# Kernel tuning notes

Measured on AMD Instinct MI355X. Metric: run time of the kernel, lower is better.

Reference implementation:

```python
import jax, jax.numpy as jnp
import numpy as np

B, N, D = 4, 4096, 512
E = 4 * D            # expanded_dim = 2048
TAIL = E // 2        # tail_dim = 1024
HALF = TAIL // 2     # mt_half = 512
HEAD = E - TAIL      # head_dim = 1024
EPS_RMS = 1e-6
EPS_NORM = 1e-12


def setup_inputs() -> dict:
    key = jax.random.key(0)
    k = jax.random.split(key, 6)
    x = jax.random.normal(k[0], (B, N, D), dtype=jnp.float32)
    g = jnp.ones((D,), dtype=jnp.float32)                                   # RMSNorm gain
    W1 = jax.random.normal(k[1], (D, E), dtype=jnp.float32) * 0.02          # Enricher linear
    b1 = jnp.zeros((E,), dtype=jnp.float32)
    V = jax.random.normal(k[2], (N, N), dtype=jnp.float32) * 0.02           # learned positional matrix slice
    bias = jnp.zeros((HALF,), dtype=jnp.float32)                            # contextualizer bias
    Wf = jax.random.normal(k[3], (HEAD + HALF, D), dtype=jnp.float32) * 0.02  # Fuser linear (no bias)
    return {"x": x, "g": g, "W1": W1, "b1": b1, "V": V, "bias": bias, "Wf": Wf}


def reference(x, g, W1, b1, V, bias, Wf):
    # RMSNorm
    xn = x * jax.lax.rsqrt(jnp.mean(jnp.square(x), axis=-1, keepdims=True) + EPS_RMS) * g
    # Enricher: relu(linear)^2
    enriched = jnp.square(jax.nn.relu(xn @ W1 + b1))                        # [B, N, E]
    head = enriched[..., :HEAD]                                             # [B, N, HEAD]
    tail = enriched[..., HEAD:]                                             # [B, N, TAIL]
    # Contextualizer
    x_left = tail[..., :HALF]
    x_right = tail[..., HALF:]
    nrm = jnp.sqrt(jnp.sum(jnp.square(x_right), axis=-1, keepdims=True))
    xr_n = x_right / jnp.maximum(nrm, EPS_NORM)                             # F.normalize, p=2
    cos = jnp.einsum('bnd,bmd->bnm', xr_n, xr_n)                            # [B, N, N] cosine sim
    weighted = V[None, :, :] * cos                                          # elementwise learned V
    ctx = jnp.einsum('bnm,bmd->bnd', weighted, xr_n)                        # chunked-path bmm uses x_right_norm
    ctx = jax.nn.sigmoid(ctx + bias)
    gated = x_left * ctx                                                    # [B, N, HALF]
    # Fuser + residual
    out = jnp.concatenate([head, gated], axis=-1) @ Wf                      # [B, N, D]
    return x + out
```

## Files before the change

### kernel.cpp

```cpp
#include <hip/hip_runtime.h>
#include <hip/hip_bf16.h>
#include <stdint.h>

typedef unsigned short u16;
typedef unsigned long long u64;
typedef __attribute__((ext_vector_type(8))) short bf16x8;
typedef __attribute__((ext_vector_type(4))) float f32x4;
typedef __attribute__((ext_vector_type(16))) float f32x16;
typedef __attribute__((ext_vector_type(4))) unsigned int u32x4;
typedef __attribute__((ext_vector_type(4))) unsigned short u16x4;

#define DEV static __device__ __forceinline__

DEV u16 f2bf(float f){
  __hip_bfloat16 h = __float2bfloat16(f);
  return __builtin_bit_cast(u16, h);
}
DEV float bf2f(u16 v){
  unsigned u = ((unsigned)v) << 16;
  return __builtin_bit_cast(float, u);
}

DEV void async_lds16(const void* g, void* l){
  __builtin_amdgcn_global_load_lds(
      (const __attribute__((address_space(1))) unsigned int*)g,
      (__attribute__((address_space(3))) unsigned int*)l, 16, 0, 0);
}

DEV f32x4 mfma16(bf16x8 a, bf16x8 b, f32x4 c){
  return __builtin_amdgcn_mfma_f32_16x16x32_bf16(a, b, c, 0, 0, 0);
}
DEV f32x16 mfma32(bf16x8 a, bf16x8 b, f32x16 c){
  return __builtin_amdgcn_mfma_f32_32x32x16_bf16(a, b, c, 0, 0, 0);
}

__global__ __launch_bounds__(64) void k_rms(const float* __restrict__ x,
                                            const float* __restrict__ g,
                                            u16* __restrict__ xn){
  const int row = blockIdx.x;
  const int l = threadIdx.x;
  const float* xr = x + (size_t)row * 512 + l * 8;
  f32x4 a = *(const f32x4*)xr;
  f32x4 c = *(const f32x4*)(xr + 4);
  float s = a[0]*a[0]+a[1]*a[1]+a[2]*a[2]+a[3]*a[3]
          + c[0]*c[0]+c[1]*c[1]+c[2]*c[2]+c[3]*c[3];
  #pragma unroll
  for (int off = 32; off >= 1; off >>= 1) s += __shfl_xor(s, off);
  float sc = rsqrtf(s * (1.f/512.f) + 1e-6f);
  f32x4 g0 = *(const f32x4*)&g[l*8];
  f32x4 g1 = *(const f32x4*)&g[l*8+4];
  u32x4 o;
  o[0] = (unsigned)f2bf(a[0]*sc*g0[0]) | ((unsigned)f2bf(a[1]*sc*g0[1]) << 16);
  o[1] = (unsigned)f2bf(a[2]*sc*g0[2]) | ((unsigned)f2bf(a[3]*sc*g0[3]) << 16);
  o[2] = (unsigned)f2bf(c[0]*sc*g1[0]) | ((unsigned)f2bf(c[1]*sc*g1[1]) << 16);
  o[3] = (unsigned)f2bf(c[2]*sc*g1[2]) | ((unsigned)f2bf(c[3]*sc*g1[3]) << 16);
  *(u32x4*)&xn[(size_t)row*512 + l*8] = o;
}

__global__ __launch_bounds__(64) void k_norm(const float* __restrict__ xr_in,
                                             u16* __restrict__ xrn){
  const int row = blockIdx.x;
  const int l = threadIdx.x;
  const float* xr = xr_in + (size_t)row * 512 + l * 8;
  f32x4 a = *(const f32x4*)xr;
  f32x4 c = *(const f32x4*)(xr + 4);
  float s = a[0]*a[0]+a[1]*a[1]+a[2]*a[2]+a[3]*a[3]
          + c[0]*c[0]+c[1]*c[1]+c[2]*c[2]+c[3]*c[3];
  #pragma unroll
  for (int off = 32; off >= 1; off >>= 1) s += __shfl_xor(s, off);
  float sc = 1.f / fmaxf(sqrtf(s), 1e-12f);
  u32x4 o;
  o[0] = (unsigned)f2bf(a[0]*sc) | ((unsigned)f2bf(a[1]*sc) << 16);
  o[1] = (unsigned)f2bf(a[2]*sc) | ((unsigned)f2bf(a[3]*sc) << 16);
  o[2] = (unsigned)f2bf(c[0]*sc) | ((unsigned)f2bf(c[1]*sc) << 16);
  o[3] = (unsigned)f2bf(c[2]*sc) | ((unsigned)f2bf(c[3]*sc) << 16);
  *(u32x4*)&xrn[(size_t)row*512 + l*8] = o;
}

__global__ __launch_bounds__(256) void k_castV(const float* __restrict__ V,
                                               u16* __restrict__ Vb){
  size_t i = ((size_t)blockIdx.x * 256 + threadIdx.x) * 8;
  f32x4 a = *(const f32x4*)&V[i];
  f32x4 c = *(const f32x4*)&V[i+4];
  u32x4 o;
  o[0] = (unsigned)f2bf(a[0]) | ((unsigned)f2bf(a[1]) << 16);
  o[1] = (unsigned)f2bf(a[2]) | ((unsigned)f2bf(a[3]) << 16);
  o[2] = (unsigned)f2bf(c[0]) | ((unsigned)f2bf(c[1]) << 16);
  o[3] = (unsigned)f2bf(c[2]) | ((unsigned)f2bf(c[3]) << 16);
  *(u32x4*)&Vb[i] = o;
}

__global__ __launch_bounds__(256) void k_tr32(const float* __restrict__ in,
                                              u16* __restrict__ out, int R, int C){
  __shared__ float tile[32][33];
  const int t = threadIdx.x;
  const int r = t >> 3;
  const int c4 = (t & 7) << 2;
  const int r0 = blockIdx.y << 5, c0 = blockIdx.x << 5;
  f32x4 v = *(const f32x4*)&in[(size_t)(r0 + r) * C + c0 + c4];
  tile[r][c4+0]=v[0]; tile[r][c4+1]=v[1]; tile[r][c4+2]=v[2]; tile[r][c4+3]=v[3];
  __syncthreads();
  u64 o =
      (u64)f2bf(tile[c4+0][r])
    | ((u64)f2bf(tile[c4+1][r]) << 16)
    | ((u64)f2bf(tile[c4+2][r]) << 32)
    | ((u64)f2bf(tile[c4+3][r]) << 48);
  *(u64*)&out[(size_t)(c0 + r) * R + r0 + c4] = o;
}

__global__ __launch_bounds__(256) void k_trb(const u16* __restrict__ in,
                                             u16* __restrict__ out, int R, int C){
  __shared__ u16 tile[32][40];
  const int t = threadIdx.x;
  const int r = t >> 3;
  const int c4 = (t & 7) << 2;
  const size_t bb = (size_t)blockIdx.z * R * C;
  const int r0 = blockIdx.y << 5, c0 = blockIdx.x << 5;
  u64 v = *(const u64*)&in[bb + (size_t)(r0 + r)*C + c0 + c4];
  tile[r][c4+0]=(u16)v; tile[r][c4+1]=(u16)(v>>16);
  tile[r][c4+2]=(u16)(v>>32); tile[r][c4+3]=(u16)(v>>48);
  __syncthreads();
  u64 o =
      (u64)tile[c4+0][r]
    | ((u64)tile[c4+1][r] << 16)
    | ((u64)tile[c4+2][r] << 32)
    | ((u64)tile[c4+3][r] << 48);
  *(u64*)&out[bb + (size_t)(c0 + r) * R + r0 + c4] = o;
}

__global__ __launch_bounds__(256) void k_gemm1(const u16* __restrict__ A,
                                               const u16* __restrict__ Bt,
                                               const float* __restrict__ b1,
                                               u16* __restrict__ head,
                                               float* __restrict__ xleft,
                                               float* __restrict__ xright){
  __shared__ u16 As[128*32];
  __shared__ u16 Bs[128*32];
  const int t = threadIdx.x;
  const int l = t & 63;
  const int w = t >> 6;
  const int wr = w >> 1, wc = w & 1;
  const int m0 = blockIdx.x << 7;
  const int n0 = blockIdx.y << 7;
  const int ra = t >> 2;
  const int kb = (t & 3) << 3;
  const int lr = l & 15, lh = l >> 4;
  f32x4 acc[4][4];
  #pragma unroll
  for (int i=0;i<4;i++)
    #pragma unroll
    for (int j=0;j<4;j++)
      #pragma unroll
      for (int r=0;r<4;r++) acc[i][j][r] = 0.f;
  for (int k0 = 0; k0 < 512; k0 += 32){
    async_lds16(A  + (size_t)(m0 + ra)*512      + k0 + kb, &As[t*8]);
    async_lds16(A  + (size_t)(m0 + 64 + ra)*512 + k0 + kb, &As[2048 + t*8]);
    async_lds16(Bt + (size_t)(n0 + ra)*512      + k0 + kb, &Bs[t*8]);
    async_lds16(Bt + (size_t)(n0 + 64 + ra)*512 + k0 + kb, &Bs[2048 + t*8]);
    __syncthreads();
    bf16x8 af[4], bfr[4];
    #pragma unroll
    for (int i=0;i<4;i++){
      af[i]  = *(const bf16x8*)&As[(wr*64 + i*16 + lr)*32 + lh*8];
      bfr[i] = *(const bf16x8*)&Bs[(wc*64 + i*16 + lr)*32 + lh*8];
    }
    #pragma unroll
    for (int i=0;i<4;i++)
      #pragma unroll
      for (int j=0;j<4;j++)
        acc[i][j] = mfma16(af[i], bfr[j], acc[i][j]);
    __syncthreads();
  }
  #pragma unroll
  for (int i=0;i<4;i++){
    #pragma unroll
    for (int j=0;j<4;j++){
      int c = n0 + wc*64 + j*16 + lr;
      float bb = b1[c];
      #pragma unroll
      for (int r=0;r<4;r++){
        int m = m0 + wr*64 + i*16 + lh*4 + r;
        float v = acc[i][j][r] + bb;
        v = v > 0.f ? v*v : 0.f;
        if (c < 1024)      head[(size_t)m*1024 + c] = f2bf(v);
        else if (c < 1536) xleft[(size_t)m*512 + (c - 1024)] = v;
        else               xright[(size_t)m*512 + (c - 1536)] = v;
      }
    }
  }
}

__global__ __launch_bounds__(256) void k_gemm3(const u16* __restrict__ head,
                                               const u16* __restrict__ gated,
                                               const u16* __restrict__ Wft,
                                               const float* __restrict__ x,
                                               float* __restrict__ out){
  __shared__ u16 As[128*32];
  __shared__ u16 Bs[128*32];
  const int t = threadIdx.x;
  const int l = t & 63;
  const int w = t >> 6;
  const int wr = w >> 1, wc = w & 1;
  const int m0 = blockIdx.x << 7;
  const int n0 = blockIdx.y << 7;
  const int ra = t >> 2;
  const int kb = (t & 3) << 3;
  const int lr = l & 15, lh = l >> 4;
  f32x4 acc[4][4];
  #pragma unroll
  for (int i=0;i<4;i++)
    #pragma unroll
    for (int j=0;j<4;j++)
      #pragma unroll
      for (int r=0;r<4;r++) acc[i][j][r] = 0.f;
  for (int k0 = 0; k0 < 1536; k0 += 32){
    const u16* sa; size_t lda; int kk;
    if (k0 < 1024){ sa = head;  lda = 1024; kk = k0; }
    else          { sa = gated; lda = 512;  kk = k0 - 1024; }
    async_lds16(sa + (size_t)(m0 + ra)*lda      + kk + kb, &As[t*8]);
    async_lds16(sa + (size_t)(m0 + 64 + ra)*lda + kk + kb, &As[2048 + t*8]);
    async_lds16(Wft + (size_t)(n0 + ra)*1536      + k0 + kb, &Bs[t*8]);
    async_lds16(Wft + (size_t)(n0 + 64 + ra)*1536 + k0 + kb, &Bs[2048 + t*8]);
    __syncthreads();
    bf16x8 af[4], bfr[4];
    #pragma unroll
    for (int i=0;i<4;i++){
      af[i]  = *(const bf16x8*)&As[(wr*64 + i*16 + lr)*32 + lh*8];
      bfr[i] = *(const bf16x8*)&Bs[(wc*64 + i*16 + lr)*32 + lh*8];
    }
    #pragma unroll
    for (int i=0;i<4;i++)
      #pragma unroll
      for (int j=0;j<4;j++)
        acc[i][j] = mfma16(af[i], bfr[j], acc[i][j]);
    __syncthreads();
  }
  #pragma unroll
  for (int i=0;i<4;i++){
    #pragma unroll
    for (int j=0;j<4;j++){
      int c = n0 + wc*64 + j*16 + lr;
      #pragma unroll
      for (int r=0;r<4;r++){
        int m = m0 + wr*64 + i*16 + lh*4 + r;
        size_t gi = (size_t)m*512 + c;
        out[gi] = x[gi] + acc[i][j][r];
      }
    }
  }
}

__global__ __launch_bounds__(512, 2) void k_attn(const u16* __restrict__ xrn,
                                                 const u16* __restrict__ xrT,
                                                 const u16* __restrict__ Vb,
                                                 const float* __restrict__ bias,
                                                 const float* __restrict__ xleft,
                                                 u16* __restrict__ gated){
  __shared__ char smem[153600];
  char* km = smem;
  char* tq = smem + 65536;
  char* ps = smem + 131072;
  char* pb = smem + 149504;
  const int t = threadIdx.x;
  const int l = t & 63, w = t >> 6;
  const int wr = w >> 2, ks = w & 3, wc = (w >> 1) & 1, kq2 = w & 1;
  const int lo = l & 31, hi = l >> 5;
  const int bid = blockIdx.x;
  const int b  = (bid & 7) >> 1;
  const int n0 = ((((bid >> 3) << 1) | (bid & 1))) << 6;
  const u16* xb  = xrn + (size_t)b * (4096*512);
  const u16* xTb = xrT + (size_t)b * (512*4096);

  bf16x8 areg[8];
  {
    const u16* apt = xb + (size_t)(n0 + wr*32 + lo)*512 + ks*128 + hi*8;
    #pragma unroll
    for (int kq = 0; kq < 8; ++kq) areg[kq] = *(const bf16x8*)(apt + kq*16);
  }
  f32x16 acc[8];
  #pragma unroll
  for (int i = 0; i < 8; ++i)
    #pragma unroll
    for (int j = 0; j < 16; ++j) acc[i][j] = 0.f;

  const int prf = t >> 3;
  const int pc4 = (t & 7) << 2;
  const int wrr = prf >> 5, prr = prf & 31;

  #pragma unroll
  for (int c = 0; c < 4; ++c){
    int off = (c*512 + t)*16;
    int row = off >> 10, colb = off & 1023;
    async_lds16(xb + (size_t)row*512 + ((colb ^ ((row&15)<<4)) >> 1), km + off);
    int r   = off >> 8;
    int lg  = (off & 255) ^ ((r & 15) << 4);
    int q   = lg >> 6;
    int mc  = (lg & 63) >> 1;
    async_lds16(xTb + (size_t)(q*128 + r)*4096 + mc, tq + off);
  }
  __syncthreads();

  int cur = 0;
  for (int it = 0; it < 128; ++it){
    const int m0 = it << 5;
    u16x4 vv = *(const u16x4*)&Vb[(size_t)(n0 + prf)*4096 + m0 + pc4];
    if (it < 127){
      const int m1 = m0 + 32;
      const int nb = (cur ^ 1) * 32768;
      #pragma unroll
      for (int c = 0; c < 4; ++c){
        int off = (c*512 + t)*16;
        int row = off >> 10, colb = off & 1023;
        async_lds16(xb + (size_t)(m1 + row)*512 + ((colb ^ ((row&15)<<4)) >> 1),
                    km + nb + off);
        int r   = off >> 8;
        int lg  = (off & 255) ^ ((r & 15) << 4);
        int q   = lg >> 6;
        int mc  = (lg & 63) >> 1;
        async_lds16(xTb + (size_t)(q*128 + r)*4096 + m1 + mc, tq + nb + off);
      }
    }
    f32x16 S0, S1;
    #pragma unroll
    for (int j = 0; j < 16; ++j){ S0[j] = 0.f; S1[j] = 0.f; }
    {
      const char* kbp = km + cur*32768 + lo*1024;
      const int swk = (lo & 15) << 4;
      __builtin_amdgcn_s_setprio(1);
      #pragma unroll
      for (int kq = 0; kq < 8; kq += 2){
        bf16x8 b0 = *(const bf16x8*)(kbp + ((ks*256 + kq*32 + hi*16) ^ swk));
        bf16x8 b1 = *(const bf16x8*)(kbp + ((ks*256 + (kq+1)*32 + hi*16) ^ swk));
        S0 = mfma32(areg[kq],   b0, S0);
        S1 = mfma32(areg[kq+1], b1, S1);
      }
      __builtin_amdgcn_s_setprio(0);
    }
    {
      char* pw = ps + ((wr*4 + ks)*32)*72 + lo*2;
      #pragma unroll
      for (int rg = 0; rg < 16; ++rg){
        int prow = (rg & 3) + 8*(rg >> 2) + 4*hi;
        *(u16*)(pw + prow*72) = f2bf(S0[rg] + S1[rg]);
      }
    }
    asm volatile("s_waitcnt lgkmcnt(0)" ::: "memory");
    __builtin_amdgcn_s_barrier();
    __builtin_amdgcn_sched_barrier(0);
    {
      float s0=0.f, s1=0.f, s2=0.f, s3=0.f;
      #pragma unroll
      for (int k2 = 0; k2 < 4; ++k2){
        u16x4 pv = *(const u16x4*)(ps + (((wrr*4 + k2)*32 + prr)*36 + pc4)*2);
        s0 += bf2f(pv[0]); s1 += bf2f(pv[1]); s2 += bf2f(pv[2]); s3 += bf2f(pv[3]);
      }
      u64 po = (u64)f2bf(s0 * bf2f(vv[0]))
             | ((u64)f2bf(s1 * bf2f(vv[1])) << 16)
             | ((u64)f2bf(s2 * bf2f(vv[2])) << 32)
             | ((u64)f2bf(s3 * bf2f(vv[3])) << 48);
      *(u64*)(pb + prf*72 + pc4*2) = po;
    }
    asm volatile("s_waitcnt lgkmcnt(0)" ::: "memory");
    __builtin_amdgcn_s_barrier();
    __builtin_amdgcn_sched_barrier(0);
    {
      bf16x8 pa = *(const bf16x8*)(pb + (wr*32 + lo)*72 + kq2*32 + hi*16);
      const char* tb = tq + cur*32768;
      __builtin_amdgcn_s_setprio(1);
      #pragma unroll
      for (int ds = 0; ds < 8; ++ds){
        int d = wc*256 + ds*32 + lo;
        int r = d & 127, q = d >> 7;
        bf16x8 bfr = *(const bf16x8*)(tb + r*256 +
                       ((q*64 + kq2*32 + hi*16) ^ ((r & 15) << 4)));
        acc[ds] = mfma32(pa, bfr, acc[ds]);
      }
      __builtin_amdgcn_s_setprio(0);
    }
    __syncthreads();
    cur ^= 1;
  }

  float* red = (float*)smem;
  const int rbase = (wr*2 + wc) * 8192;
  if (kq2 == 1){
    #pragma unroll
    for (int ds = 0; ds < 8; ++ds)
      #pragma unroll
      for (int rg = 0; rg < 16; ++rg)
        red[rbase + (ds*16 + rg)*64 + l] = acc[ds][rg];
  }
  __syncthreads();
  if (kq2 == 0){
    #pragma unroll
    for (int ds = 0; ds < 8; ++ds){
      const int d = wc*256 + ds*32 + lo;
      const float bs = bias[d];
      #pragma unroll
      for (int rg = 0; rg < 16; ++rg){
        int row = n0 + wr*32 + (rg & 3) + 8*(rg >> 2) + 4*hi;
        float v = acc[ds][rg] + red[rbase + (ds*16 + rg)*64 + l] + bs;
        v = 1.f / (1.f + __expf(-v));
        size_t gi = (size_t)(b*4096 + row)*512 + d;
        gated[gi] = f2bf(xleft[gi] * v);
      }
    }
  }
}

extern "C" void kernel_launch(void* const* d_in, const int* in_sizes, int n_in,
                              void* d_out, int out_size, void* d_ws, size_t ws_size,
                              hipStream_t stream){
  const float* x    = (const float*)d_in[0];
  const float* g    = (const float*)d_in[1];
  const float* W1   = (const float*)d_in[2];
  const float* b1   = (const float*)d_in[3];
  const float* V    = (const float*)d_in[4];
  const float* bias = (const float*)d_in[5];
  const float* Wf   = (const float*)d_in[6];
  float* out = (float*)d_out;

  char* ws = (char*)d_ws;
  const size_t MB = 1024u*1024u;
  u16*   xn     = (u16*)  (ws + 0*MB);
  u16*   W1t    = (u16*)  (ws + 16*MB);
  u16*   Vbf    = (u16*)  (ws + 0*MB);
  u16*   Wft    = (u16*)  (ws + 32*MB);
  u16*   head   = (u16*)  (ws + 34*MB);
  float* xleft  = (float*)(ws + 66*MB);
  float* xright = (float*)(ws + 98*MB);
  u16*   gated  = (u16*)  (ws + 98*MB);
  u16*   xrn    = (u16*)  (ws + 130*MB);
  u16*   xrT    = (u16*)  (ws + 146*MB);

  k_rms  <<<dim3(16384),      dim3(64),  0, stream>>>(x, g, xn);
  k_tr32 <<<dim3(64, 16),     dim3(256), 0, stream>>>(W1, W1t, 512, 2048);
  k_tr32 <<<dim3(16, 48),     dim3(256), 0, stream>>>(Wf, Wft, 1536, 512);
  k_gemm1<<<dim3(128, 16),    dim3(256), 0, stream>>>(xn, W1t, b1, head, xleft, xright);
  k_castV<<<dim3(8192),       dim3(256), 0, stream>>>(V, Vbf);
  k_norm <<<dim3(16384),      dim3(64),  0, stream>>>(xright, xrn);
  k_trb  <<<dim3(16, 128, 4), dim3(256), 0, stream>>>(xrn, xrT, 4096, 512);
  k_attn <<<dim3(256),        dim3(512), 0, stream>>>(xrn, xrT, Vbf, bias, xleft, gated);
  k_gemm3<<<dim3(128, 4),     dim3(256), 0, stream>>>(head, gated, Wft, x, out);
}
```

Measured before the change: 426.0 us.

## Fuse V bf16 cast into attention kernel and drop setprio hints

Removes the separate k_castV pass that turned the 4096x4096 V matrix into bf16, and has k_attn read fp32 V directly, multiplying in fp32 before rounding. This saves one launch and a full read/write of V, but the attention kernel now loads twice as many bytes of V per iteration. It also replaces the HIP bf16 conversion with a hand-written round-to-nearest-even bit trick, drops the s_setprio hints around the MFMA loops, compacts the workspace layout, and enlarges the shared buffer slightly.

```diff
diff --git a/kernel.cpp b/kernel.cpp
--- a/kernel.cpp
+++ b/kernel.cpp
@@ -1,5 +1,4 @@
 #include <hip/hip_runtime.h>
-#include <hip/hip_bf16.h>
 #include <stdint.h>
 
 typedef unsigned short u16;
@@ -13,8 +12,9 @@
 #define DEV static __device__ __forceinline__
 
 DEV u16 f2bf(float f){
-  __hip_bfloat16 h = __float2bfloat16(f);
-  return __builtin_bit_cast(u16, h);
+  unsigned u = __builtin_bit_cast(unsigned, f);
+  u += 0x7fffu + ((u >> 16) & 1u);
+  return (u16)(u >> 16);
 }
 DEV float bf2f(u16 v){
   unsigned u = ((unsigned)v) << 16;
@@ -75,19 +75,6 @@
   o[2] = (unsigned)f2bf(c[0]*sc) | ((unsigned)f2bf(c[1]*sc) << 16);
   o[3] = (unsigned)f2bf(c[2]*sc) | ((unsigned)f2bf(c[3]*sc) << 16);
   *(u32x4*)&xrn[(size_t)row*512 + l*8] = o;
-}
-
-__global__ __launch_bounds__(256) void k_castV(const float* __restrict__ V,
-                                               u16* __restrict__ Vb){
-  size_t i = ((size_t)blockIdx.x * 256 + threadIdx.x) * 8;
-  f32x4 a = *(const f32x4*)&V[i];
-  f32x4 c = *(const f32x4*)&V[i+4];
-  u32x4 o;
-  o[0] = (unsigned)f2bf(a[0]) | ((unsigned)f2bf(a[1]) << 16);
-  o[1] = (unsigned)f2bf(a[2]) | ((unsigned)f2bf(a[3]) << 16);
-  o[2] = (unsigned)f2bf(c[0]) | ((unsigned)f2bf(c[1]) << 16);
-  o[3] = (unsigned)f2bf(c[2]) | ((unsigned)f2bf(c[3]) << 16);
-  *(u32x4*)&Vb[i] = o;
 }
 
 __global__ __launch_bounds__(256) void k_tr32(const float* __restrict__ in,
@@ -252,11 +239,11 @@
 
 __global__ __launch_bounds__(512, 2) void k_attn(const u16* __restrict__ xrn,
                                                  const u16* __restrict__ xrT,
-                                                 const u16* __restrict__ Vb,
+                                                 const float* __restrict__ V,
                                                  const float* __restrict__ bias,
                                                  const float* __restrict__ xleft,
                                                  u16* __restrict__ gated){
-  __shared__ char smem[153600];
+  __shared__ char smem[154624];
   char* km = smem;
   char* tq = smem + 65536;
   char* ps = smem + 131072;
@@ -303,7 +290,7 @@
   int cur = 0;
   for (int it = 0; it < 128; ++it){
     const int m0 = it << 5;
-    u16x4 vv = *(const u16x4*)&Vb[(size_t)(n0 + prf)*4096 + m0 + pc4];
+    f32x4 vf = *(const f32x4*)&V[(size_t)(n0 + prf)*4096 + m0 + pc4];
     if (it < 127){
       const int m1 = m0 + 32;
       const int nb = (cur ^ 1) * 32768;
@@ -326,7 +313,6 @@
     {
       const char* kbp = km + cur*32768 + lo*1024;
       const int swk = (lo & 15) << 4;
-      __builtin_amdgcn_s_setprio(1);
       #pragma unroll
       for (int kq = 0; kq < 8; kq += 2){
         bf16x8 b0 = *(const bf16x8*)(kbp + ((ks*256 + kq*32 + hi*16) ^ swk));
@@ -334,7 +320,6 @@
         S0 = mfma32(areg[kq],   b0, S0);
         S1 = mfma32(areg[kq+1], b1, S1);
       }
-      __builtin_amdgcn_s_setprio(0);
     }
     {
       char* pw = ps + ((wr*4 + ks)*32)*72 + lo*2;
@@ -354,10 +339,10 @@
         u16x4 pv = *(const u16x4*)(ps + (((wrr*4 + k2)*32 + prr)*36 + pc4)*2);
         s0 += bf2f(pv[0]); s1 += bf2f(pv[1]); s2 += bf2f(pv[2]); s3 += bf2f(pv[3]);
       }
-      u64 po = (u64)f2bf(s0 * bf2f(vv[0]))
-             | ((u64)f2bf(s1 * bf2f(vv[1])) << 16)
-             | ((u64)f2bf(s2 * bf2f(vv[2])) << 32)
-             | ((u64)f2bf(s3 * bf2f(vv[3])) << 48);
+      u64 po = (u64)f2bf(s0 * vf[0])
+             | ((u64)f2bf(s1 * vf[1]) << 16)
+             | ((u64)f2bf(s2 * vf[2]) << 32)
+             | ((u64)f2bf(s3 * vf[3]) << 48);
       *(u64*)(pb + prf*72 + pc4*2) = po;
     }
     asm volatile("s_waitcnt lgkmcnt(0)" ::: "memory");
@@ -366,7 +351,6 @@
     {
       bf16x8 pa = *(const bf16x8*)(pb + (wr*32 + lo)*72 + kq2*32 + hi*16);
       const char* tb = tq + cur*32768;
-      __builtin_amdgcn_s_setprio(1);
       #pragma unroll
       for (int ds = 0; ds < 8; ++ds){
         int d = wc*256 + ds*32 + lo;
@@ -375,7 +359,6 @@
                        ((q*64 + kq2*32 + hi*16) ^ ((r & 15) << 4)));
         acc[ds] = mfma32(pa, bfr, acc[ds]);
       }
-      __builtin_amdgcn_s_setprio(0);
     }
     __syncthreads();
     cur ^= 1;
@@ -424,22 +407,20 @@
   const size_t MB = 1024u*1024u;
   u16*   xn     = (u16*)  (ws + 0*MB);
   u16*   W1t    = (u16*)  (ws + 16*MB);
-  u16*   Vbf    = (u16*)  (ws + 0*MB);
-  u16*   Wft    = (u16*)  (ws + 32*MB);
-  u16*   head   = (u16*)  (ws + 34*MB);
-  float* xleft  = (float*)(ws + 66*MB);
-  float* xright = (float*)(ws + 98*MB);
-  u16*   gated  = (u16*)  (ws + 98*MB);
-  u16*   xrn    = (u16*)  (ws + 130*MB);
-  u16*   xrT    = (u16*)  (ws + 146*MB);
+  u16*   Wft    = (u16*)  (ws + 18*MB);
+  u16*   head   = (u16*)  (ws + 20*MB);
+  float* xleft  = (float*)(ws + 52*MB);
+  float* xright = (float*)(ws + 84*MB);
+  u16*   gated  = (u16*)  (ws + 84*MB);
+  u16*   xrn    = (u16*)  (ws + 116*MB);
+  u16*   xrT    = (u16*)  (ws + 132*MB);
 
   k_rms  <<<dim3(16384),      dim3(64),  0, stream>>>(x, g, xn);
   k_tr32 <<<dim3(64, 16),     dim3(256), 0, stream>>>(W1, W1t, 512, 2048);
   k_tr32 <<<dim3(16, 48),     dim3(256), 0, stream>>>(Wf, Wft, 1536, 512);
   k_gemm1<<<dim3(128, 16),    dim3(256), 0, stream>>>(xn, W1t, b1, head, xleft, xright);
-  k_castV<<<dim3(8192),       dim3(256), 0, stream>>>(V, Vbf);
   k_norm <<<dim3(16384),      dim3(64),  0, stream>>>(xright, xrn);
   k_trb  <<<dim3(16, 128, 4), dim3(256), 0, stream>>>(xrn, xrT, 4096, 512);
-  k_attn <<<dim3(256),        dim3(512), 0, stream>>>(xrn, xrT, Vbf, bias, xleft, gated);
+  k_attn <<<dim3(256),        dim3(512), 0, stream>>>(xrn, xrT, V, bias, xleft, gated);
   k_gemm3<<<dim3(128, 4),     dim3(256), 0, stream>>>(head, gated, Wft, x, out);
 }
```

New measurement: 404.0 us. 1.05x faster.
